# Optimization experiments

Hardware: AMD Instinct MI355X
Metric: run time of the kernel (lower is better)

Reference implementation:

```python
import jax, jax.numpy as jnp
import numpy as np

N_NODES = 100000


def setup_inputs() -> dict:
    key = jax.random.key(0)
    k1, k2, k3, k4 = jax.random.split(key, 4)
    x = jax.random.normal(k1, (N_NODES, 64), dtype=jnp.float32)
    W = jax.random.normal(k2, (64, 64), dtype=jnp.float32) * (1.0 / np.sqrt(64.0))
    src = jax.random.randint(k3, (1600000,), 0, N_NODES, dtype=jnp.int32)
    dst = jax.random.randint(k4, (1600000,), 0, N_NODES, dtype=jnp.int32)
    return {"x": x, "W": W, "src": src, "dst": dst}


def reference(x, W, src, dst):
    n = x.shape[0]
    ones = jnp.ones(src.shape[0], dtype=x.dtype)
    out_deg = jax.ops.segment_sum(ones, src, num_segments=n)  # out-degree of each node
    in_deg = jax.ops.segment_sum(ones, dst, num_segments=n)   # in-degree of each node
    norm_src = jnp.power(jnp.clip(out_deg, 1.0, None), -0.5)  # D_out^{-1/2}, clamp(min=1)
    norm_dst = jnp.power(jnp.clip(in_deg, 1.0, None), -0.5)   # D_in^{-1/2}, clamp(min=1)
    # in_feats == out_feats -> DGL aggregates first, then applies the weight
    feat = x * norm_src[:, None]                              # [N, d_in]
    msgs = feat[src]                                          # [E, d_in] gather
    agg = jax.ops.segment_sum(msgs, dst, num_segments=n)      # [N, d_in] scatter-add
    agg = agg * norm_dst[:, None]
    return agg @ W                                            # [N, d_out]
```

## Files before the change

kernel.cpp:

```cpp
#include <hip/hip_runtime.h>
#include <math.h>

#define D 64
#define SCAN_TILE 1024
#define SCAN_THREADS 256
#define SCAN_ITEMS 4
#define HS 16
#define BSHIFT 9
#define BW 512
#define CHUNK 2048

__device__ __forceinline__ unsigned pack_bf16(float a, float b) {
    unsigned ua = __float_as_uint(a);
    unsigned ub = __float_as_uint(b);
    ua = (ua + 0x7fffu + ((ua >> 16) & 1u)) >> 16;
    ub = (ub + 0x7fffu + ((ub >> 16) & 1u)) >> 16;
    return ua | (ub << 16);
}
__device__ __forceinline__ float blo(unsigned u) { return __uint_as_float(u << 16); }
__device__ __forceinline__ float bhi(unsigned u) { return __uint_as_float(u & 0xffff0000u); }


__global__ __launch_bounds__(256)
void bucket_count_chunks2_kernel(const int* __restrict__ src, const int* __restrict__ dst,
                                 int* __restrict__ bcnt_d, int* __restrict__ bcnt_s,
                                 int E, int NBv) {
    __shared__ int cd[256];
    __shared__ int cs[256];
    for (int i = threadIdx.x; i < NBv; i += 256) { cd[i] = 0; cs[i] = 0; }
    __syncthreads();
    int beg = blockIdx.x * CHUNK;
    int end = beg + CHUNK; if (end > E) end = E;
    for (int j = beg + threadIdx.x; j < end; j += 256) {
        atomicAdd(&cd[dst[j] >> BSHIFT], 1);
        atomicAdd(&cs[src[j] >> BSHIFT], 1);
    }
    __syncthreads();
    for (int i = threadIdx.x; i < NBv; i += 256) {
        bcnt_d[(size_t)blockIdx.x * NBv + i] = cd[i];
        bcnt_s[(size_t)blockIdx.x * NBv + i] = cs[i];
    }
}

__global__ __launch_bounds__(256)
void bucket_scan_chunks2_kernel(const int* __restrict__ bcnt_d, int* __restrict__ bstart_d,
                                int* __restrict__ btot_d,
                                const int* __restrict__ bcnt_s, int* __restrict__ bstart_s,
                                int* __restrict__ btot_s,
                                int nChunks, int NBv) {
    __shared__ int sdata[256];
    int which = (blockIdx.x >= NBv) ? 1 : 0;
    int b = blockIdx.x - which * NBv;
    const int* bcnt   = which ? bcnt_s : bcnt_d;
    int*       bstart = which ? bstart_s : bstart_d;
    int*       btot   = which ? btot_s : btot_d;
    int t = threadIdx.x;
    int carry = 0;
    for (int c0 = 0; c0 < nChunks; c0 += 256) {
        int c = c0 + t;
        int v = (c < nChunks) ? bcnt[(size_t)c * NBv + b] : 0;
        sdata[t] = v;
        __syncthreads();
        for (int off = 1; off < 256; off <<= 1) {
            int val = (t >= off) ? sdata[t - off] : 0;
            __syncthreads();
            if (t >= off) sdata[t] += val;
            __syncthreads();
        }
        if (c < nChunks) bstart[(size_t)c * NBv + b] = carry + sdata[t] - v;
        carry += sdata[255];
        __syncthreads();
    }
    if (t == 0) btot[b] = carry;
}

__global__ __launch_bounds__(256)
void bucket_base2_kernel(const int* __restrict__ btot_d, int* __restrict__ bbeg_d,
                         const int* __restrict__ btot_s, int* __restrict__ bbeg_s,
                         int NBv, int E) {
    __shared__ int sdata[256];
    const int* btot = (blockIdx.x == 0) ? btot_d : btot_s;
    int*       bbeg = (blockIdx.x == 0) ? bbeg_d : bbeg_s;
    int t = threadIdx.x;
    int v = (t < NBv) ? btot[t] : 0;
    sdata[t] = v;
    __syncthreads();
    for (int off = 1; off < 256; off <<= 1) {
        int val = (t >= off) ? sdata[t - off] : 0;
        __syncthreads();
        if (t >= off) sdata[t] += val;
        __syncthreads();
    }
    if (t < NBv) bbeg[t] = sdata[t] - v;
    if (t == 0) bbeg[NBv] = E;
}

__global__ __launch_bounds__(256)
void bucket_scatter2_kernel(const int* __restrict__ src, const int* __restrict__ dst,
                            const int* __restrict__ bstart_d, const int* __restrict__ bbeg_d,
                            const int* __restrict__ bstart_s, const int* __restrict__ bbeg_s,
                            unsigned* __restrict__ bucketed_d,
                            unsigned short* __restrict__ bucketed_s,
                            int E, int NBv) {
    __shared__ int cur_d[256];
    __shared__ int cur_s[256];
    for (int i = threadIdx.x; i < NBv; i += 256) {
        cur_d[i] = bstart_d[(size_t)blockIdx.x * NBv + i] + bbeg_d[i];
        cur_s[i] = bstart_s[(size_t)blockIdx.x * NBv + i] + bbeg_s[i];
    }
    __syncthreads();
    int beg = blockIdx.x * CHUNK;
    int end = beg + CHUNK; if (end > E) end = E;
    for (int j = beg + threadIdx.x; j < end; j += 256) {
        int d = dst[j];
        int s = src[j];
        int pd = atomicAdd(&cur_d[d >> BSHIFT], 1);
        bucketed_d[pd] = ((unsigned)(d & (BW - 1)) << 17) | (unsigned)s;
        int ps = atomicAdd(&cur_s[s >> BSHIFT], 1);
        bucketed_s[ps] = (unsigned short)(s & (BW - 1));
    }
}

__global__ __launch_bounds__(256)
void bucket_finalize_kernel(const unsigned* __restrict__ bucketed_d,
                            const int* __restrict__ bbeg_d,
                            const unsigned short* __restrict__ bucketed_s,
                            const int* __restrict__ bbeg_s,
                            int* __restrict__ offsets, float* __restrict__ norm_dst,
                            float* __restrict__ norm_src, int* __restrict__ sorted_src,
                            int N, int E, int NBv) {
    __shared__ int cnt[BW];
    __shared__ int cur[BW];
    __shared__ int ssum[256];
    int t = threadIdx.x;
    if (blockIdx.x < NBv) {
        int b = blockIdx.x;
        cnt[t] = 0; cnt[t + 256] = 0;
        __syncthreads();
        int beg = bbeg_d[b], end = bbeg_d[b + 1];
        for (int j = beg + t; j < end; j += 256)
            atomicAdd(&cnt[bucketed_d[j] >> 17], 1);
        __syncthreads();
        int c0 = cnt[2 * t], c1 = cnt[2 * t + 1];
        ssum[t] = c0 + c1;
        __syncthreads();
        for (int off = 1; off < 256; off <<= 1) {
            int v = (t >= off) ? ssum[t - off] : 0;
            __syncthreads();
            if (t >= off) ssum[t] += v;
            __syncthreads();
        }
        int excl = ssum[t] - (c0 + c1);
        int off0 = beg + excl;
        int off1 = off0 + c0;
        int dbase = b << BSHIFT;
        int d0 = dbase + 2 * t, d1 = dbase + 2 * t + 1;
        cur[2 * t] = off0; cur[2 * t + 1] = off1;
        if (d0 < N) {
            offsets[d0] = off0;
            norm_dst[d0] = 1.0f / sqrtf((float)(c0 < 1 ? 1 : c0));
        }
        if (d1 < N) {
            offsets[d1] = off1;
            norm_dst[d1] = 1.0f / sqrtf((float)(c1 < 1 ? 1 : c1));
        }
        if (b == NBv - 1 && t == 0) offsets[N] = E;
        __syncthreads();
        for (int j = beg + t; j < end; j += 256) {
            unsigned v = bucketed_d[j];
            int pos = atomicAdd(&cur[v >> 17], 1);
            sorted_src[pos] = (int)(v & 0x1FFFFu);
        }
    } else {
        int b = blockIdx.x - NBv;
        cnt[t] = 0; cnt[t + 256] = 0;
        __syncthreads();
        int beg = bbeg_s[b], end = bbeg_s[b + 1];
        for (int j = beg + t; j < end; j += 256)
            atomicAdd(&cnt[bucketed_s[j]], 1);
        __syncthreads();
        int sbase = b << BSHIFT;
        for (int i = t; i < BW; i += 256) {
            int s = sbase + i;
            if (s < N) {
                int c = cnt[i];
                norm_src[s] = 1.0f / sqrtf((float)(c < 1 ? 1 : c));
            }
        }
    }
}


__global__ __launch_bounds__(SCAN_THREADS)
void scan_blocks_kernel(const int* __restrict__ cnt_dst, int* __restrict__ offsets,
                        int* __restrict__ partials, int N, int S) {
    __shared__ int sdata[SCAN_THREADS];
    int t = threadIdx.x;
    int base = blockIdx.x * SCAN_TILE + t * SCAN_ITEMS;
    int v[SCAN_ITEMS];
    int sum = 0;
    #pragma unroll
    for (int i = 0; i < SCAN_ITEMS; ++i) {
        int idx = base + i;
        v[i] = (idx < N) ? cnt_dst[(size_t)idx * S] : 0;
        sum += v[i];
    }
    sdata[t] = sum;
    __syncthreads();
    for (int off = 1; off < SCAN_THREADS; off <<= 1) {
        int val = (t >= off) ? sdata[t - off] : 0;
        __syncthreads();
        if (t >= off) sdata[t] += val;
        __syncthreads();
    }
    int excl = sdata[t] - sum;
    if (t == SCAN_THREADS - 1) partials[blockIdx.x] = sdata[t];
    int run = excl;
    #pragma unroll
    for (int i = 0; i < SCAN_ITEMS; ++i) {
        int idx = base + i;
        if (idx < N) offsets[idx] = run;
        run += v[i];
    }
}

__global__ __launch_bounds__(SCAN_THREADS)
void scan_partials_kernel(int* __restrict__ partials, int nblk) {
    __shared__ int sdata[SCAN_THREADS];
    int t = threadIdx.x;
    int v = (t < nblk) ? partials[t] : 0;
    sdata[t] = v;
    __syncthreads();
    for (int off = 1; off < SCAN_THREADS; off <<= 1) {
        int val = (t >= off) ? sdata[t - off] : 0;
        __syncthreads();
        if (t >= off) sdata[t] += val;
        __syncthreads();
    }
    if (t < nblk) partials[t] = sdata[t] - v;
}

__global__ void add_back_kernel(int* __restrict__ offsets, int* __restrict__ cursor,
                                const int* __restrict__ partials, int N, int E, int S) {
    int i = blockIdx.x * blockDim.x + threadIdx.x;
    if (i < N) {
        int o = offsets[i] + partials[i >> 10];
        offsets[i] = o;
        cursor[(size_t)i * S] = o;
    }
    if (i == 0) offsets[N] = E;
}


#define XW_ROWS 64
#define ATP 68

__global__ __launch_bounds__(256, 4)
void xw_tiled_kernel(const float4* __restrict__ x4, const float* __restrict__ W,
                     const float* __restrict__ norm_src, unsigned* __restrict__ y, int N) {
    __shared__ float Ws[D * D];
    __shared__ float At[D][ATP];
    int t = threadIdx.x;

    for (int i = t; i < D * D / 4; i += 256)
        reinterpret_cast<float4*>(Ws)[i] = reinterpret_cast<const float4*>(W)[i];

    int rowbase = blockIdx.x * XW_ROWS;
    int lr = t >> 2;
    int qc = t & 3;
    int gr = rowbase + lr;
    float ns = (gr < N) ? norm_src[gr] : 0.0f;
    #pragma unroll
    for (int c = qc; c < 16; c += 4) {
        float4 v = (gr < N) ? x4[(size_t)gr * 16 + c] : make_float4(0.f, 0.f, 0.f, 0.f);
        At[c * 4 + 0][lr] = v.x * ns;
        At[c * 4 + 1][lr] = v.y * ns;
        At[c * 4 + 2][lr] = v.z * ns;
        At[c * 4 + 3][lr] = v.w * ns;
    }
    __syncthreads();

    int tx = t & 15;
    int ty = t >> 4;
    float4 acc0 = make_float4(0.f, 0.f, 0.f, 0.f);
    float4 acc1 = acc0, acc2 = acc0, acc3 = acc0;
    #pragma unroll 4
    for (int k = 0; k < D; ++k) {
        float4 a = *reinterpret_cast<const float4*>(&At[k][ty * 4]);
        float4 w = *reinterpret_cast<const float4*>(&Ws[k * D + tx * 4]);
        acc0.x += a.x * w.x; acc0.y += a.x * w.y; acc0.z += a.x * w.z; acc0.w += a.x * w.w;
        acc1.x += a.y * w.x; acc1.y += a.y * w.y; acc1.z += a.y * w.z; acc1.w += a.y * w.w;
        acc2.x += a.z * w.x; acc2.y += a.z * w.y; acc2.z += a.z * w.z; acc2.w += a.z * w.w;
        acc3.x += a.w * w.x; acc3.y += a.w * w.y; acc3.z += a.w * w.z; acc3.w += a.w * w.w;
    }

    uint2* y2 = reinterpret_cast<uint2*>(y);
    int r0 = rowbase + ty * 4;
    if (r0 + 0 < N) y2[(size_t)(r0 + 0) * 16 + tx] =
        make_uint2(pack_bf16(acc0.x, acc0.y), pack_bf16(acc0.z, acc0.w));
    if (r0 + 1 < N) y2[(size_t)(r0 + 1) * 16 + tx] =
        make_uint2(pack_bf16(acc1.x, acc1.y), pack_bf16(acc1.z, acc1.w));
    if (r0 + 2 < N) y2[(size_t)(r0 + 2) * 16 + tx] =
        make_uint2(pack_bf16(acc2.x, acc2.y), pack_bf16(acc2.z, acc2.w));
    if (r0 + 3 < N) y2[(size_t)(r0 + 3) * 16 + tx] =
        make_uint2(pack_bf16(acc3.x, acc3.y), pack_bf16(acc3.z, acc3.w));
}


__global__ __launch_bounds__(256)
void agg_bf16_kernel(const uint4* __restrict__ y4, const int* __restrict__ offsets,
                     const int* __restrict__ sorted_src, const float* __restrict__ norm_dst,
                     float4* __restrict__ out4, int N) {
    int wave = (blockIdx.x << 2) + (threadIdx.x >> 6);
    if (wave >= N) return;
    int lane = threadIdx.x & 63;
    int g = lane >> 3;
    int q = lane & 7;
    int beg = offsets[wave];
    int end = offsets[wave + 1];
    float nd = norm_dst[wave];
    float a0 = 0.f, a1 = 0.f, a2 = 0.f, a3 = 0.f, a4 = 0.f, a5 = 0.f, a6 = 0.f, a7 = 0.f;
    int j = beg + g;
    while (j + 8 < end) {
        int s0 = sorted_src[j];
        int s1 = sorted_src[j + 8];
        uint4 v0 = y4[(size_t)s0 * 8 + q];
        uint4 v1 = y4[(size_t)s1 * 8 + q];
        a0 += blo(v0.x) + blo(v1.x); a1 += bhi(v0.x) + bhi(v1.x);
        a2 += blo(v0.y) + blo(v1.y); a3 += bhi(v0.y) + bhi(v1.y);
        a4 += blo(v0.z) + blo(v1.z); a5 += bhi(v0.z) + bhi(v1.z);
        a6 += blo(v0.w) + blo(v1.w); a7 += bhi(v0.w) + bhi(v1.w);
        j += 16;
    }
    if (j < end) {
        int s = sorted_src[j];
        uint4 v = y4[(size_t)s * 8 + q];
        a0 += blo(v.x); a1 += bhi(v.x);
        a2 += blo(v.y); a3 += bhi(v.y);
        a4 += blo(v.z); a5 += bhi(v.z);
        a6 += blo(v.w); a7 += bhi(v.w);
    }
    a0 += __shfl_xor(a0, 8);  a1 += __shfl_xor(a1, 8);
    a2 += __shfl_xor(a2, 8);  a3 += __shfl_xor(a3, 8);
    a4 += __shfl_xor(a4, 8);  a5 += __shfl_xor(a5, 8);
    a6 += __shfl_xor(a6, 8);  a7 += __shfl_xor(a7, 8);
    a0 += __shfl_xor(a0, 16); a1 += __shfl_xor(a1, 16);
    a2 += __shfl_xor(a2, 16); a3 += __shfl_xor(a3, 16);
    a4 += __shfl_xor(a4, 16); a5 += __shfl_xor(a5, 16);
    a6 += __shfl_xor(a6, 16); a7 += __shfl_xor(a7, 16);
    a0 += __shfl_xor(a0, 32); a1 += __shfl_xor(a1, 32);
    a2 += __shfl_xor(a2, 32); a3 += __shfl_xor(a3, 32);
    a4 += __shfl_xor(a4, 32); a5 += __shfl_xor(a5, 32);
    a6 += __shfl_xor(a6, 32); a7 += __shfl_xor(a7, 32);
    if (lane < 8) {
        float4 o1; o1.x = a0 * nd; o1.y = a1 * nd; o1.z = a2 * nd; o1.w = a3 * nd;
        float4 o2; o2.x = a4 * nd; o2.y = a5 * nd; o2.z = a6 * nd; o2.w = a7 * nd;
        out4[(size_t)wave * 16 + q * 2]     = o1;
        out4[(size_t)wave * 16 + q * 2 + 1] = o2;
    }
}


__global__ void hist4_kernel(const int* __restrict__ src, const int* __restrict__ dst,
                             int* __restrict__ cnt, int E, int N, int S) {
    int i = blockIdx.x * blockDim.x + threadIdx.x;
    int E4 = E >> 2;
    if (i < E4) {
        int4 s = reinterpret_cast<const int4*>(src)[i];
        int4 d = reinterpret_cast<const int4*>(dst)[i];
        atomicAdd(&cnt[s.x * S], 1); atomicAdd(&cnt[s.y * S], 1);
        atomicAdd(&cnt[s.z * S], 1); atomicAdd(&cnt[s.w * S], 1);
        atomicAdd(&cnt[(N + d.x) * S], 1); atomicAdd(&cnt[(N + d.y) * S], 1);
        atomicAdd(&cnt[(N + d.z) * S], 1); atomicAdd(&cnt[(N + d.w) * S], 1);
    }
    if (i == 0) {
        for (int e = E4 << 2; e < E; ++e) {
            atomicAdd(&cnt[src[e] * S], 1);
            atomicAdd(&cnt[(N + dst[e]) * S], 1);
        }
    }
}

__global__ void norm_from_cnt_kernel(const int* __restrict__ cnt, float* __restrict__ norm,
                                     int twoN, int S) {
    int i = blockIdx.x * blockDim.x + threadIdx.x;
    if (i < twoN) {
        int c = cnt[(size_t)i * S];
        float v = (float)(c < 1 ? 1 : c);
        norm[i] = 1.0f / sqrtf(v);
    }
}

__global__ void bin4_kernel(const int* __restrict__ src, const int* __restrict__ dst,
                            int* __restrict__ cursor, int* __restrict__ sorted_src,
                            int E, int S) {
    int i = blockIdx.x * blockDim.x + threadIdx.x;
    int E4 = E >> 2;
    if (i < E4) {
        int4 s = reinterpret_cast<const int4*>(src)[i];
        int4 d = reinterpret_cast<const int4*>(dst)[i];
        sorted_src[atomicAdd(&cursor[d.x * S], 1)] = s.x;
        sorted_src[atomicAdd(&cursor[d.y * S], 1)] = s.y;
        sorted_src[atomicAdd(&cursor[d.z * S], 1)] = s.z;
        sorted_src[atomicAdd(&cursor[d.w * S], 1)] = s.w;
    }
    if (i == 0) {
        for (int e = E4 << 2; e < E; ++e) {
            sorted_src[atomicAdd(&cursor[dst[e] * S], 1)] = src[e];
        }
    }
}

__global__ void deg_kernel(const int* __restrict__ src, const int* __restrict__ dst,
                           float* __restrict__ deg, int E, int N) {
    int i = blockIdx.x * blockDim.x + threadIdx.x;
    if (i < E) {
        atomicAdd(&deg[src[i]], 1.0f);
        atomicAdd(&deg[N + dst[i]], 1.0f);
    }
}

__global__ void norm_kernel(float* __restrict__ deg, int twoN) {
    int i = blockIdx.x * blockDim.x + threadIdx.x;
    if (i < twoN) {
        float v = deg[i];
        v = v < 1.0f ? 1.0f : v;
        deg[i] = 1.0f / sqrtf(v);
    }
}

__global__ void scatter_kernel(const float* __restrict__ x, const int* __restrict__ src,
                               const int* __restrict__ dst, const float* __restrict__ norm_src,
                               float* __restrict__ agg, int E) {
    int tid = blockIdx.x * blockDim.x + threadIdx.x;
    int e = tid >> 4;
    int q = tid & 15;
    if (e < E) {
        int s = src[e];
        int d = dst[e];
        float ns = norm_src[s];
        float4 v = reinterpret_cast<const float4*>(x)[s * (D / 4) + q];
        float* o = agg + (long long)d * D + q * 4;
        atomicAdd(o + 0, v.x * ns);
        atomicAdd(o + 1, v.y * ns);
        atomicAdd(o + 2, v.z * ns);
        atomicAdd(o + 3, v.w * ns);
    }
}

__global__ __launch_bounds__(256) void gemm_kernel(float* __restrict__ out,
                                                   const float* __restrict__ W,
                                                   const float* __restrict__ norm_dst,
                                                   int N, int rows_per_block) {
    __shared__ float Ws[D * D];
    __shared__ float rowS[4][D];
    for (int i = threadIdx.x; i < D * D; i += 256) Ws[i] = W[i];

    int f   = threadIdx.x & 63;
    int sub = threadIdx.x >> 6;
    int base = blockIdx.x * rows_per_block;

    for (int r0 = 0; r0 < rows_per_block; r0 += 4) {
        int r = base + r0 + sub;
        bool valid = (r < N);
        __syncthreads();
        if (valid) rowS[sub][f] = out[(long long)r * D + f] * norm_dst[r];
        __syncthreads();
        if (valid) {
            float acc = 0.0f;
            #pragma unroll
            for (int k = 0; k < D; ++k) acc += rowS[sub][k] * Ws[k * D + f];
            out[(long long)r * D + f] = acc;
        }
    }
}

extern "C" void kernel_launch(void* const* d_in, const int* in_sizes, int n_in,
                              void* d_out, int out_size, void* d_ws, size_t ws_size,
                              hipStream_t stream) {
    const float* x   = (const float*)d_in[0];
    const float* W   = (const float*)d_in[1];
    const int*   src = (const int*)d_in[2];
    const int*   dst = (const int*)d_in[3];

    const int N = in_sizes[0] / D;
    const int E = in_sizes[2];
    const int nblk = (N + SCAN_TILE - 1) / SCAN_TILE;
    const int NBv = (N + BW - 1) >> BSHIFT;
    const int nChunks = (E + CHUNK - 1) / CHUNK;

    size_t w_norm = 0;
    size_t w_offs = w_norm + 2 * (size_t)N;
    size_t w_bcd  = w_offs + (size_t)N + 1;
    size_t w_bsd  = w_bcd + (size_t)nChunks * NBv;
    size_t w_bcs  = w_bsd + (size_t)nChunks * NBv;
    size_t w_bss  = w_bcs + (size_t)nChunks * NBv;
    size_t w_btd  = w_bss + (size_t)nChunks * NBv;
    size_t w_bbd  = w_btd + (size_t)NBv;
    size_t w_bts  = w_bbd + (size_t)NBv + 1;
    size_t w_bbs  = w_bts + (size_t)NBv;
    size_t w_bkd  = w_bbs + (size_t)NBv + 1;
    size_t w_bks  = w_bkd + (size_t)E;
    size_t w_sort = w_bks + ((size_t)E + 1) / 2;
    size_t w_y    = (w_sort + (size_t)E + 3) & ~(size_t)3;
    size_t need_new = (w_y + (size_t)N * 32) * 4;

    bool new_ok = (N <= (1 << 17)) && (NBv <= 256) && (ws_size >= need_new);

    if (new_ok) {
        float*          norm       = (float*)d_ws + w_norm;
        int*            offsets    = (int*)d_ws + w_offs;
        int*            bcnt_d     = (int*)d_ws + w_bcd;
        int*            bstart_d   = (int*)d_ws + w_bsd;
        int*            bcnt_s     = (int*)d_ws + w_bcs;
        int*            bstart_s   = (int*)d_ws + w_bss;
        int*            btot_d     = (int*)d_ws + w_btd;
        int*            bbeg_d     = (int*)d_ws + w_bbd;
        int*            btot_s     = (int*)d_ws + w_bts;
        int*            bbeg_s     = (int*)d_ws + w_bbs;
        unsigned*       bucketed_d = (unsigned*)d_ws + w_bkd;
        unsigned short* bucketed_s = (unsigned short*)((int*)d_ws + w_bks);
        int*            sorted_src = (int*)d_ws + w_sort;
        unsigned*       y          = (unsigned*)d_ws + w_y;
        float*          out        = (float*)d_out;

        bucket_count_chunks2_kernel<<<nChunks, 256, 0, stream>>>(src, dst, bcnt_d, bcnt_s,
                                                                 E, NBv);
        bucket_scan_chunks2_kernel<<<2 * NBv, 256, 0, stream>>>(bcnt_d, bstart_d, btot_d,
                                                                bcnt_s, bstart_s, btot_s,
                                                                nChunks, NBv);
        bucket_base2_kernel<<<2, 256, 0, stream>>>(btot_d, bbeg_d, btot_s, bbeg_s, NBv, E);
        bucket_scatter2_kernel<<<nChunks, 256, 0, stream>>>(src, dst, bstart_d, bbeg_d,
                                                            bstart_s, bbeg_s, bucketed_d,
                                                            bucketed_s, E, NBv);
        bucket_finalize_kernel<<<2 * NBv, 256, 0, stream>>>(bucketed_d, bbeg_d,
                                                            bucketed_s, bbeg_s,
                                                            offsets, norm + N, norm,
                                                            sorted_src, N, E, NBv);

        xw_tiled_kernel<<<(N + XW_ROWS - 1) / XW_ROWS, 256, 0, stream>>>(
            (const float4*)x, W, norm, y, N);
        int agg_blocks = (N + 3) / 4;
        agg_bf16_kernel<<<agg_blocks, 256, 0, stream>>>(
            (const uint4*)y, offsets, sorted_src, norm + N, (float4*)out, N);
        return;
    }

    {
        const int strides[4] = {16, 8, 4, 1};
        int S = 0;
        size_t o_norm = 0, o_cnt = 0, o_offs = 0, o_cur = 0, o_part = 0, o_sort = 0, o_yy = 0;
        size_t need_A = 0;
        for (int t = 0; t < 4; ++t) {
            int s = strides[t];
            o_norm = 0;
            o_cnt  = o_norm + 2 * (size_t)N;
            o_offs = o_cnt + 2 * (size_t)N * s;
            o_cur  = o_offs + (size_t)N + 1;
            o_part = o_cur + (size_t)N * s;
            o_sort = o_part + SCAN_THREADS;
            o_yy   = (o_sort + (size_t)E + 3) & ~(size_t)3;
            need_A = (o_yy + (size_t)N * 32) * 4;
            if (ws_size >= need_A) { S = s; break; }
        }
        if (S > 0 && nblk <= SCAN_THREADS) {
            float*    norm       = (float*)d_ws + o_norm;
            int*      cnt        = (int*)d_ws + o_cnt;
            int*      offsets    = (int*)d_ws + o_offs;
            int*      cursor     = (int*)d_ws + o_cur;
            int*      partials   = (int*)d_ws + o_part;
            int*      sorted_src = (int*)d_ws + o_sort;
            unsigned* y          = (unsigned*)d_ws + o_yy;
            float*    out        = (float*)d_out;

            hipMemsetAsync(cnt, 0, 2 * (size_t)N * S * sizeof(int), stream);

            int E4 = E >> 2;
            int histblk = (E4 + 255) / 256; if (histblk < 1) histblk = 1;
            hist4_kernel<<<histblk, 256, 0, stream>>>(src, dst, cnt, E, N, S);
            norm_from_cnt_kernel<<<(2 * N + 255) / 256, 256, 0, stream>>>(cnt, norm, 2 * N, S);
            scan_blocks_kernel<<<nblk, SCAN_THREADS, 0, stream>>>(cnt + (size_t)N * S, offsets,
                                                                  partials, N, S);
            scan_partials_kernel<<<1, SCAN_THREADS, 0, stream>>>(partials, nblk);
            add_back_kernel<<<(N + 255) / 256, 256, 0, stream>>>(offsets, cursor, partials,
                                                                 N, E, S);
            bin4_kernel<<<histblk, 256, 0, stream>>>(src, dst, cursor, sorted_src, E, S);

            xw_tiled_kernel<<<(N + XW_ROWS - 1) / XW_ROWS, 256, 0, stream>>>(
                (const float4*)x, W, norm, y, N);
            int agg_blocks = (N + 3) / 4;
            agg_bf16_kernel<<<agg_blocks, 256, 0, stream>>>(
                (const uint4*)y, offsets, sorted_src, norm + N, (float4*)out, N);
            return;
        }
    }

    {
        float* deg = (float*)d_ws;
        float* agg = (float*)d_out;

        hipMemsetAsync(deg, 0, (size_t)2 * N * sizeof(float), stream);
        hipMemsetAsync(agg, 0, (size_t)N * D * sizeof(float), stream);

        deg_kernel<<<(E + 255) / 256, 256, 0, stream>>>(src, dst, deg, E, N);
        norm_kernel<<<(2 * N + 255) / 256, 256, 0, stream>>>(deg, 2 * N);

        long long scatter_threads = (long long)E * 16;
        int scatter_blocks = (int)((scatter_threads + 255) / 256);
        scatter_kernel<<<scatter_blocks, 256, 0, stream>>>(x, src, dst, deg, agg, E);

        const int rows_per_block = 64;
        int gemm_blocks = (N + rows_per_block - 1) / rows_per_block;
        gemm_kernel<<<gemm_blocks, 256, 0, stream>>>(agg, W, deg + N, N, rows_per_block);
    }
}
```

Baseline: 142.7 us.

## Replace per-chunk bucket scan with atomic reservation and add thread-per-row aggregation

The bucket sort drops the per-chunk count matrix and its scan kernel. Chunk counts are now added atomically into padded global totals. The scatter kernel recounts its chunk and reserves space with one global atomicAdd per bucket, which removes a kernel launch and the count and offset buffers but reads the edge arrays an extra time. A new aggregation kernel gives each thread one destination row and one quarter of the feature columns. It is used when the bf16 feature table is small enough to likely stay in L2, and trades coalescing within a wave for fewer reductions and more rows in flight.

New measurement: 310.0 us. 2.17x slower.

```diff
diff --git a/kernel.cpp b/kernel.cpp
--- a/kernel.cpp
+++ b/kernel.cpp
@@ -9,6 +9,7 @@
 #define BSHIFT 9
 #define BW 512
 #define CHUNK 2048
+#define CP 16
 
 __device__ __forceinline__ unsigned pack_bf16(float a, float b) {
     unsigned ua = __float_as_uint(a);
@@ -22,9 +23,9 @@
 
 
 __global__ __launch_bounds__(256)
-void bucket_count_chunks2_kernel(const int* __restrict__ src, const int* __restrict__ dst,
-                                 int* __restrict__ bcnt_d, int* __restrict__ bcnt_s,
-                                 int E, int NBv) {
+void count_chunks_kernel(const int* __restrict__ src, const int* __restrict__ dst,
+                         int* __restrict__ btot_d, int* __restrict__ btot_s,
+                         int E, int NBv) {
     __shared__ int cd[256];
     __shared__ int cs[256];
     for (int i = threadIdx.x; i < NBv; i += 256) { cd[i] = 0; cs[i] = 0; }
@@ -37,52 +38,22 @@
     }
     __syncthreads();
     for (int i = threadIdx.x; i < NBv; i += 256) {
-        bcnt_d[(size_t)blockIdx.x * NBv + i] = cd[i];
-        bcnt_s[(size_t)blockIdx.x * NBv + i] = cs[i];
+        if (cd[i]) atomicAdd(&btot_d[i * CP], cd[i]);
+        if (cs[i]) atomicAdd(&btot_s[i * CP], cs[i]);
     }
 }
 
 __global__ __launch_bounds__(256)
-void bucket_scan_chunks2_kernel(const int* __restrict__ bcnt_d, int* __restrict__ bstart_d,
-                                int* __restrict__ btot_d,
-                                const int* __restrict__ bcnt_s, int* __restrict__ bstart_s,
-                                int* __restrict__ btot_s,
-                                int nChunks, int NBv) {
-    __shared__ int sdata[256];
-    int which = (blockIdx.x >= NBv) ? 1 : 0;
-    int b = blockIdx.x - which * NBv;
-    const int* bcnt   = which ? bcnt_s : bcnt_d;
-    int*       bstart = which ? bstart_s : bstart_d;
-    int*       btot   = which ? btot_s : btot_d;
-    int t = threadIdx.x;
-    int carry = 0;
-    for (int c0 = 0; c0 < nChunks; c0 += 256) {
-        int c = c0 + t;
-        int v = (c < nChunks) ? bcnt[(size_t)c * NBv + b] : 0;
-        sdata[t] = v;
-        __syncthreads();
-        for (int off = 1; off < 256; off <<= 1) {
-            int val = (t >= off) ? sdata[t - off] : 0;
-            __syncthreads();
-            if (t >= off) sdata[t] += val;
-            __syncthreads();
-        }
-        if (c < nChunks) bstart[(size_t)c * NBv + b] = carry + sdata[t] - v;
-        carry += sdata[255];
-        __syncthreads();
-    }
-    if (t == 0) btot[b] = carry;
-}
-
-__global__ __launch_bounds__(256)
-void bucket_base2_kernel(const int* __restrict__ btot_d, int* __restrict__ bbeg_d,
-                         const int* __restrict__ btot_s, int* __restrict__ bbeg_s,
-                         int NBv, int E) {
+void base_init_kernel(const int* __restrict__ btot_d, int* __restrict__ bbeg_d,
+                      int* __restrict__ gcur_d,
+                      const int* __restrict__ btot_s, int* __restrict__ bbeg_s,
+                      int* __restrict__ gcur_s, int NBv, int E) {
     __shared__ int sdata[256];
     const int* btot = (blockIdx.x == 0) ? btot_d : btot_s;
     int*       bbeg = (blockIdx.x == 0) ? bbeg_d : bbeg_s;
+    int*       gcur = (blockIdx.x == 0) ? gcur_d : gcur_s;
     int t = threadIdx.x;
-    int v = (t < NBv) ? btot[t] : 0;
+    int v = (t < NBv) ? btot[t * CP] : 0;
     sdata[t] = v;
     __syncthreads();
     for (int off = 1; off < 256; off <<= 1) {
@@ -91,26 +62,38 @@
         if (t >= off) sdata[t] += val;
         __syncthreads();
     }
-    if (t < NBv) bbeg[t] = sdata[t] - v;
+    if (t < NBv) {
+        int base = sdata[t] - v;
+        bbeg[t] = base;
+        gcur[t * CP] = base;
+    }
     if (t == 0) bbeg[NBv] = E;
 }
 
 __global__ __launch_bounds__(256)
-void bucket_scatter2_kernel(const int* __restrict__ src, const int* __restrict__ dst,
-                            const int* __restrict__ bstart_d, const int* __restrict__ bbeg_d,
-                            const int* __restrict__ bstart_s, const int* __restrict__ bbeg_s,
+void scatter_reserve_kernel(const int* __restrict__ src, const int* __restrict__ dst,
+                            int* __restrict__ gcur_d, int* __restrict__ gcur_s,
                             unsigned* __restrict__ bucketed_d,
                             unsigned short* __restrict__ bucketed_s,
                             int E, int NBv) {
+    __shared__ int cd[256];
+    __shared__ int cs[256];
     __shared__ int cur_d[256];
     __shared__ int cur_s[256];
-    for (int i = threadIdx.x; i < NBv; i += 256) {
-        cur_d[i] = bstart_d[(size_t)blockIdx.x * NBv + i] + bbeg_d[i];
-        cur_s[i] = bstart_s[(size_t)blockIdx.x * NBv + i] + bbeg_s[i];
-    }
+    for (int i = threadIdx.x; i < NBv; i += 256) { cd[i] = 0; cs[i] = 0; }
     __syncthreads();
     int beg = blockIdx.x * CHUNK;
     int end = beg + CHUNK; if (end > E) end = E;
+    for (int j = beg + threadIdx.x; j < end; j += 256) {
+        atomicAdd(&cd[dst[j] >> BSHIFT], 1);
+        atomicAdd(&cs[src[j] >> BSHIFT], 1);
+    }
+    __syncthreads();
+    for (int i = threadIdx.x; i < NBv; i += 256) {
+        cur_d[i] = cd[i] ? atomicAdd(&gcur_d[i * CP], cd[i]) : 0;
+        cur_s[i] = cs[i] ? atomicAdd(&gcur_s[i * CP], cs[i]) : 0;
+    }
+    __syncthreads();
     for (int j = beg + threadIdx.x; j < end; j += 256) {
         int d = dst[j];
         int s = src[j];
@@ -304,6 +287,59 @@
         make_uint2(pack_bf16(acc2.x, acc2.y), pack_bf16(acc2.z, acc2.w));
     if (r0 + 3 < N) y2[(size_t)(r0 + 3) * 16 + tx] =
         make_uint2(pack_bf16(acc3.x, acc3.y), pack_bf16(acc3.z, acc3.w));
+}
+
+
+__global__ __launch_bounds__(256)
+void agg_slice_kernel(const uint4* __restrict__ y4, const int* __restrict__ offsets,
+                      const int* __restrict__ sorted_src, const float* __restrict__ norm_dst,
+                      float4* __restrict__ out4, int N) {
+    int q0 = blockIdx.x & 3;
+    int row = (blockIdx.x >> 2) * 256 + threadIdx.x;
+    if (row >= N) return;
+    int beg = offsets[row];
+    int end = offsets[row + 1];
+    float nd = norm_dst[row];
+    float a0 = 0.f, a1 = 0.f, a2 = 0.f, a3 = 0.f, a4 = 0.f, a5 = 0.f, a6 = 0.f, a7 = 0.f;
+    float b0 = 0.f, b1 = 0.f, b2 = 0.f, b3 = 0.f, b4 = 0.f, b5 = 0.f, b6 = 0.f, b7 = 0.f;
+    int qb = 2 * q0;
+    int j = beg;
+    while (j + 1 < end) {
+        int s0 = sorted_src[j];
+        int s1 = sorted_src[j + 1];
+        uint4 u0 = y4[(size_t)s0 * 8 + qb];
+        uint4 u1 = y4[(size_t)s0 * 8 + qb + 1];
+        uint4 w0 = y4[(size_t)s1 * 8 + qb];
+        uint4 w1 = y4[(size_t)s1 * 8 + qb + 1];
+        a0 += blo(u0.x) + blo(w0.x); a1 += bhi(u0.x) + bhi(w0.x);
+        a2 += blo(u0.y) + blo(w0.y); a3 += bhi(u0.y) + bhi(w0.y);
+        a4 += blo(u0.z) + blo(w0.z); a5 += bhi(u0.z) + bhi(w0.z);
+        a6 += blo(u0.w) + blo(w0.w); a7 += bhi(u0.w) + bhi(w0.w);
+        b0 += blo(u1.x) + blo(w1.x); b1 += bhi(u1.x) + bhi(w1.x);
+        b2 += blo(u1.y) + blo(w1.y); b3 += bhi(u1.y) + bhi(w1.y);
+        b4 += blo(u1.z) + blo(w1.z); b5 += bhi(u1.z) + bhi(w1.z);
+        b6 += blo(u1.w) + blo(w1.w); b7 += bhi(u1.w) + bhi(w1.w);
+        j += 2;
+    }
+    if (j < end) {
+        int s = sorted_src[j];
+        uint4 u0 = y4[(size_t)s * 8 + qb];
+        uint4 u1 = y4[(size_t)s * 8 + qb + 1];
+        a0 += blo(u0.x); a1 += bhi(u0.x);
+        a2 += blo(u0.y); a3 += bhi(u0.y);
+        a4 += blo(u0.z); a5 += bhi(u0.z);
+        a6 += blo(u0.w); a7 += bhi(u0.w);
+        b0 += blo(u1.x); b1 += bhi(u1.x);
+        b2 += blo(u1.y); b3 += bhi(u1.y);
+        b4 += blo(u1.z); b5 += bhi(u1.z);
+        b6 += blo(u1.w); b7 += bhi(u1.w);
+    }
+    size_t ob = (size_t)row * 16 + q0 * 4;
+    float4 o;
+    o.x = a0 * nd; o.y = a1 * nd; o.z = a2 * nd; o.w = a3 * nd; out4[ob + 0] = o;
+    o.x = a4 * nd; o.y = a5 * nd; o.z = a6 * nd; o.w = a7 * nd; out4[ob + 1] = o;
+    o.x = b0 * nd; o.y = b1 * nd; o.z = b2 * nd; o.w = b3 * nd; out4[ob + 2] = o;
+    o.x = b4 * nd; o.y = b5 * nd; o.z = b6 * nd; o.w = b7 * nd; out4[ob + 3] = o;
 }
 
 
@@ -491,15 +527,13 @@
 
     size_t w_norm = 0;
     size_t w_offs = w_norm + 2 * (size_t)N;
-    size_t w_bcd  = w_offs + (size_t)N + 1;
-    size_t w_bsd  = w_bcd + (size_t)nChunks * NBv;
-    size_t w_bcs  = w_bsd + (size_t)nChunks * NBv;
-    size_t w_bss  = w_bcs + (size_t)nChunks * NBv;
-    size_t w_btd  = w_bss + (size_t)nChunks * NBv;
-    size_t w_bbd  = w_btd + (size_t)NBv;
-    size_t w_bts  = w_bbd + (size_t)NBv + 1;
-    size_t w_bbs  = w_bts + (size_t)NBv;
-    size_t w_bkd  = w_bbs + (size_t)NBv + 1;
+    size_t w_btd  = w_offs + (size_t)N + 1;
+    size_t w_bts  = w_btd + (size_t)NBv * CP;
+    size_t w_bbd  = w_bts + (size_t)NBv * CP;
+    size_t w_bbs  = w_bbd + (size_t)NBv + 1;
+    size_t w_gcd  = w_bbs + (size_t)NBv + 1;
+    size_t w_gcs  = w_gcd + (size_t)NBv * CP;
+    size_t w_bkd  = w_gcs + (size_t)NBv * CP;
     size_t w_bks  = w_bkd + (size_t)E;
     size_t w_sort = w_bks + ((size_t)E + 1) / 2;
     size_t w_y    = (w_sort + (size_t)E + 3) & ~(size_t)3;
@@ -510,29 +544,25 @@
     if (new_ok) {
         float*          norm       = (float*)d_ws + w_norm;
         int*            offsets    = (int*)d_ws + w_offs;
-        int*            bcnt_d     = (int*)d_ws + w_bcd;
-        int*            bstart_d   = (int*)d_ws + w_bsd;
-        int*            bcnt_s     = (int*)d_ws + w_bcs;
-        int*            bstart_s   = (int*)d_ws + w_bss;
         int*            btot_d     = (int*)d_ws + w_btd;
+        int*            btot_s     = (int*)d_ws + w_bts;
         int*            bbeg_d     = (int*)d_ws + w_bbd;
-        int*            btot_s     = (int*)d_ws + w_bts;
         int*            bbeg_s     = (int*)d_ws + w_bbs;
+        int*            gcur_d     = (int*)d_ws + w_gcd;
+        int*            gcur_s     = (int*)d_ws + w_gcs;
         unsigned*       bucketed_d = (unsigned*)d_ws + w_bkd;
         unsigned short* bucketed_s = (unsigned short*)((int*)d_ws + w_bks);
         int*            sorted_src = (int*)d_ws + w_sort;
         unsigned*       y          = (unsigned*)d_ws + w_y;
         float*          out        = (float*)d_out;
 
-        bucket_count_chunks2_kernel<<<nChunks, 256, 0, stream>>>(src, dst, bcnt_d, bcnt_s,
-                                                                 E, NBv);
-        bucket_scan_chunks2_kernel<<<2 * NBv, 256, 0, stream>>>(bcnt_d, bstart_d, btot_d,
-                                                                bcnt_s, bstart_s, btot_s,
-                                                                nChunks, NBv);
-        bucket_base2_kernel<<<2, 256, 0, stream>>>(btot_d, bbeg_d, btot_s, bbeg_s, NBv, E);
-        bucket_scatter2_kernel<<<nChunks, 256, 0, stream>>>(src, dst, bstart_d, bbeg_d,
-                                                            bstart_s, bbeg_s, bucketed_d,
-                                                            bucketed_s, E, NBv);
+        hipMemsetAsync(btot_d, 0, 2 * (size_t)NBv * CP * sizeof(int), stream);
+
+        count_chunks_kernel<<<nChunks, 256, 0, stream>>>(src, dst, btot_d, btot_s, E, NBv);
+        base_init_kernel<<<2, 256, 0, stream>>>(btot_d, bbeg_d, gcur_d,
+                                                btot_s, bbeg_s, gcur_s, NBv, E);
+        scatter_reserve_kernel<<<nChunks, 256, 0, stream>>>(src, dst, gcur_d, gcur_s,
+                                                            bucketed_d, bucketed_s, E, NBv);
         bucket_finalize_kernel<<<2 * NBv, 256, 0, stream>>>(bucketed_d, bbeg_d,
                                                             bucketed_s, bbeg_s,
                                                             offsets, norm + N, norm,
@@ -540,9 +570,16 @@
 
         xw_tiled_kernel<<<(N + XW_ROWS - 1) / XW_ROWS, 256, 0, stream>>>(
             (const float4*)x, W, norm, y, N);
-        int agg_blocks = (N + 3) / 4;
-        agg_bf16_kernel<<<agg_blocks, 256, 0, stream>>>(
-            (const uint4*)y, offsets, sorted_src, norm + N, (float4*)out, N);
+
+        if ((size_t)N * 32 <= (size_t)(3.5 * 1024 * 1024)) {
+            int tiles = (N + 255) / 256;
+            agg_slice_kernel<<<tiles * 4, 256, 0, stream>>>(
+                (const uint4*)y, offsets, sorted_src, norm + N, (float4*)out, N);
+        } else {
+            int agg_blocks = (N + 3) / 4;
+            agg_bf16_kernel<<<agg_blocks, 256, 0, stream>>>(
+                (const uint4*)y, offsets, sorted_src, norm + N, (float4*)out, N);
+        }
         return;
     }
 
```
